# Kernel optimization log

Measured on AMD Instinct MI355X. Metric: run time of the kernel, lower is better.

## Reference

```python
import jax, jax.numpy as jnp
import numpy as np

LEAK = 0.01  # F.leaky_relu default negative_slope


def projection(p, cam, res):
    # Weak-perspective projection to normalized [-1,1] image coords.
    # cam = [s, tx, ty]; p [B,N,3] -> [B,N,2]
    s = cam[:, 0][:, None, None]
    t = cam[:, None, 1:3]
    return s * (p[..., :2] + t)


def grid_sample_points(im_feat, pts):
    # Bilinear grid_sample with align_corners=True, zeros padding,
    # specialized to a [B,N,1,2] point grid (matches points.unsqueeze(2)).
    # im_feat [B,C,H,W], pts [B,N,2] in [-1,1] -> [B,C,N]
    B, C, H, W = im_feat.shape
    N = pts.shape[1]
    x = (pts[..., 0] + 1.0) * 0.5 * (W - 1)
    y = (pts[..., 1] + 1.0) * 0.5 * (H - 1)
    x0 = jnp.floor(x)
    y0 = jnp.floor(y)
    x1 = x0 + 1.0
    y1 = y0 + 1.0
    wx1 = x - x0
    wx0 = 1.0 - wx1
    wy1 = y - y0
    wy0 = 1.0 - wy1
    feat_flat = im_feat.reshape(B, C, H * W)

    def gather(xi, yi, w):
        valid = (xi >= 0) & (xi <= W - 1) & (yi >= 0) & (yi <= H - 1)
        xc = jnp.clip(xi, 0, W - 1).astype(jnp.int32)
        yc = jnp.clip(yi, 0, H - 1).astype(jnp.int32)
        idx = (yc * W + xc)[:, None, :]  # [B,1,N]
        g = jnp.take_along_axis(feat_flat, jnp.broadcast_to(idx, (B, C, N)), axis=2)
        return g * (w * valid.astype(w.dtype))[:, None, :]

    return (gather(x0, y0, wx0 * wy0) + gather(x1, y0, wx1 * wy0)
            + gather(x0, y1, wx0 * wy1) + gather(x1, y1, wx1 * wy1))


def reduce_dim(feat, W0, b0, W1, b1, W2, b2):
    # feat [B,C0,N]; Conv1d kernel_size=1 == channel matmul.
    def conv1x1(x, W, b):
        return jnp.einsum('oc,bcn->bon', W, x) + b[None, :, None]

    y = jax.nn.leaky_relu(conv1x1(feat, W0, b0), LEAK)
    y = jax.nn.leaky_relu(conv1x1(jnp.concatenate([y, feat], axis=1), W1, b1), LEAK)
    y = conv1x1(jnp.concatenate([y, feat], axis=1), W2, b2)
    y = jax.nn.relu(y)  # last_op
    return y.reshape(y.shape[0], -1)  # [B, C_p*N]


def setup_inputs() -> dict:
    key = jax.random.key(0)
    ks = jax.random.split(key, 9)
    B, N, C, H, Wd = 64, 431, 256, 56, 56
    dims = [256, 128, 64, 5]
    p = jax.random.normal(ks[0], (B, N, 3), jnp.float32)
    cam = jax.random.uniform(ks[1], (B, 3), jnp.float32)
    s_feat = jax.random.normal(ks[2], (B, C, H, Wd), jnp.float32)
    W0 = jax.random.normal(ks[3], (dims[1], dims[0]), jnp.float32) * 0.02
    b0 = jnp.zeros((dims[1],), jnp.float32)
    W1 = jax.random.normal(ks[4], (dims[2], dims[1] + dims[0]), jnp.float32) * 0.02
    b1 = jnp.zeros((dims[2],), jnp.float32)
    W2 = jax.random.normal(ks[5], (dims[3], dims[2] + dims[0]), jnp.float32) * 0.02
    b2 = jnp.zeros((dims[3],), jnp.float32)
    return {"p": p, "cam": cam, "s_feat": s_feat,
            "W0": W0, "b0": b0, "W1": W1, "b1": b1, "W2": W2, "b2": b2,
            "res": 224}


def reference(p, cam, s_feat, W0, b0, W1, b1, W2, b2, res):
    p2d = projection(p, cam, res)                 # [B,N,2]
    point_feat = grid_sample_points(s_feat, p2d)  # [B,C_s,N]
    return reduce_dim(point_feat, W0, b0, W1, b1, W2, b2)  # [B, C_p*N]
```

## Files before the change

kernel.cpp:

```cpp
#include <hip/hip_runtime.h>


#define B_   64
#define N_   431
#define C_   256
#define H_   56
#define W_   56
#define HW_  3136
#define PPB  16
#define NT_  27
#define NPAD (NT_ * PPB)

#define Y0S  136
#define Y1S  72

typedef __attribute__((ext_vector_type(8))) short short8;
typedef __attribute__((ext_vector_type(4))) float f32x4;

__device__ __forceinline__ ushort f2bf(float f) {
    unsigned u = __float_as_uint(f);
    u += 0x7fffu + ((u >> 16) & 1u);
    return (ushort)(u >> 16);
}
__device__ __forceinline__ uint pack2(float lo, float hi) {
    return (uint)f2bf(lo) | ((uint)f2bf(hi) << 16);
}
__device__ __forceinline__ float lo16(uint u) { return __uint_as_float(u << 16); }
__device__ __forceinline__ float hi16(uint u) { return __uint_as_float(u & 0xffff0000u); }

#define WTOT (128 * 256 + 64 * 384 + 16 * 320)
#define GB_  (B_ * 64)

__global__ __launch_bounds__(256, 6) void gather_kernel(
    const float* __restrict__ p,
    const float* __restrict__ cam,
    const float* __restrict__ sfeat,
    const float* __restrict__ W0,
    const float* __restrict__ W1,
    const float* __restrict__ W2,
    ushort* __restrict__ feat,
    ushort* __restrict__ W0b,
    ushort* __restrict__ W1b,
    ushort* __restrict__ W2p)
{
    const int bx = blockIdx.x;
    if (bx >= GB_) {
        const int t0 = (bx - GB_) * 256 + threadIdx.x;
        for (int i = t0; i < WTOT; i += 8 * 256) {
            if (i < 128 * 256) {
                W0b[i] = f2bf(W0[i]);
            } else if (i < 128 * 256 + 64 * 384) {
                const int j = i - 128 * 256;
                W1b[j] = f2bf(W1[j]);
            } else {
                const int j = i - (128 * 256 + 64 * 384);
                const int r = j / 320, c = j - r * 320;
                W2p[j] = (r < 5) ? f2bf(W2[r * 320 + c]) : (ushort)0;
            }
        }
        return;
    }

    __shared__ uint plane01[HW_];
    __shared__ uint plane23[HW_];

    const int b  = bx >> 6;
    const int cg = bx & 63;
    const int c0 = cg * 4;
    const int t  = threadIdx.x;

    {
        const float4* __restrict__ s0 = (const float4*)(sfeat + ((size_t)b * C_ + c0 + 0) * HW_);
        const float4* __restrict__ s1 = (const float4*)(sfeat + ((size_t)b * C_ + c0 + 1) * HW_);
        const float4* __restrict__ s2 = (const float4*)(sfeat + ((size_t)b * C_ + c0 + 2) * HW_);
        const float4* __restrict__ s3 = (const float4*)(sfeat + ((size_t)b * C_ + c0 + 3) * HW_);
        for (int k = t; k < HW_ / 4; k += 256) {
            const float4 a = s0[k], bb = s1[k];
            uint4 u01;
            u01.x = pack2(a.x, bb.x); u01.y = pack2(a.y, bb.y);
            u01.z = pack2(a.z, bb.z); u01.w = pack2(a.w, bb.w);
            *(uint4*)&plane01[k * 4] = u01;
            const float4 c = s2[k], d = s3[k];
            uint4 u23;
            u23.x = pack2(c.x, d.x); u23.y = pack2(c.y, d.y);
            u23.z = pack2(c.z, d.z); u23.w = pack2(c.w, d.w);
            *(uint4*)&plane23[k * 4] = u23;
        }
    }
    __syncthreads();

    const float s  = cam[b * 3 + 0];
    const float tx = cam[b * 3 + 1];
    const float ty = cam[b * 3 + 2];
    ushort* __restrict__ fdst = feat + ((size_t)b * 64 + cg) * NPAD * 4;

    for (int n = t; n < NPAD; n += 256) {
        int   i00 = 0, i10 = 0, i01 = 0, i11 = 0;
        float w00 = 0.f, w10 = 0.f, w01 = 0.f, w11 = 0.f;
        if (n < N_) {
            const float px = p[((size_t)b * N_ + n) * 3 + 0];
            const float py = p[((size_t)b * N_ + n) * 3 + 1];
            const float x = (s * (px + tx) + 1.f) * 0.5f * (float)(W_ - 1);
            const float y = (s * (py + ty) + 1.f) * 0.5f * (float)(H_ - 1);
            const float x0f = floorf(x), y0f = floorf(y);
            const float wx1 = x - x0f, wx0 = 1.f - wx1;
            const float wy1 = y - y0f, wy0 = 1.f - wy1;
            const int ix0 = (int)x0f, iy0 = (int)y0f;
            const int ix1 = ix0 + 1,  iy1 = iy0 + 1;
            const bool vx0 = (ix0 >= 0) & (ix0 <= W_ - 1);
            const bool vx1 = (ix1 >= 0) & (ix1 <= W_ - 1);
            const bool vy0 = (iy0 >= 0) & (iy0 <= H_ - 1);
            const bool vy1 = (iy1 >= 0) & (iy1 <= H_ - 1);
            const int cx0 = min(max(ix0, 0), W_ - 1);
            const int cx1 = min(max(ix1, 0), W_ - 1);
            const int cy0 = min(max(iy0, 0), H_ - 1);
            const int cy1 = min(max(iy1, 0), H_ - 1);
            w00 = (vx0 & vy0) ? wx0 * wy0 : 0.f;
            w10 = (vx1 & vy0) ? wx1 * wy0 : 0.f;
            w01 = (vx0 & vy1) ? wx0 * wy1 : 0.f;
            w11 = (vx1 & vy1) ? wx1 * wy1 : 0.f;
            i00 = cy0 * W_ + cx0;  i10 = cy0 * W_ + cx1;
            i01 = cy1 * W_ + cx0;  i11 = cy1 * W_ + cx1;
        }
        const uint a00 = plane01[i00], a10 = plane01[i10], a01 = plane01[i01], a11 = plane01[i11];
        const uint c00 = plane23[i00], c10 = plane23[i10], c01 = plane23[i01], c11 = plane23[i11];
        const float v0 = w00 * lo16(a00) + w10 * lo16(a10) + w01 * lo16(a01) + w11 * lo16(a11);
        const float v1 = w00 * hi16(a00) + w10 * hi16(a10) + w01 * hi16(a01) + w11 * hi16(a11);
        const float v2 = w00 * lo16(c00) + w10 * lo16(c10) + w01 * lo16(c01) + w11 * lo16(c11);
        const float v3 = w00 * hi16(c00) + w10 * hi16(c10) + w01 * hi16(c01) + w11 * hi16(c11);
        ushort4 r;
        r.x = f2bf(v0); r.y = f2bf(v1); r.z = f2bf(v2); r.w = f2bf(v3);
        *(ushort4*)(fdst + (size_t)n * 4) = r;
    }
}

__global__ __launch_bounds__(256, 4) void mlp_kernel(
    const ushort* __restrict__ feat,
    const ushort* __restrict__ W0b,
    const float* __restrict__ b0,
    const ushort* __restrict__ W1b,
    const float* __restrict__ b1,
    const ushort* __restrict__ W2p,
    const float* __restrict__ b2,
    float* __restrict__ out)
{
    __shared__ ushort y0_s[PPB * Y0S];
    __shared__ ushort y1_s[PPB * Y1S];

    const int tid  = threadIdx.x;
    const int w    = tid >> 6;
    const int l    = tid & 63;
    const int m    = l & 15;
    const int q    = l >> 4;
    const int tile = blockIdx.x;
    const int b    = blockIdx.y;
    const int n0   = tile * PPB;
    const int n    = n0 + m;

    const ushort* __restrict__ fb = feat + (size_t)b * 64 * NPAD * 4;
    short8 af[8];
    #pragma unroll
    for (int ks = 0; ks < 8; ++ks) {
        const int cg0 = 8 * ks + 2 * q;
        union { short8 v; uint2 u[2]; } tmp;
        tmp.u[0] = *(const uint2*)(fb + ((size_t)cg0 * NPAD + n) * 4);
        tmp.u[1] = *(const uint2*)(fb + ((size_t)(cg0 + 1) * NPAD + n) * 4);
        af[ks] = tmp.v;
    }

    {
        f32x4 acc0 = {0.f, 0.f, 0.f, 0.f};
        f32x4 acc1 = {0.f, 0.f, 0.f, 0.f};
        const ushort* __restrict__ wr0 = W0b + ((size_t)(2 * w) * 16 + m) * 256 + 8 * q;
        const ushort* __restrict__ wr1 = wr0 + 16 * 256;
        #pragma unroll
        for (int ks = 0; ks < 8; ++ks) {
            const short8 w0 = *(const short8*)(wr0 + 32 * ks);
            const short8 w1 = *(const short8*)(wr1 + 32 * ks);
            acc0 = __builtin_amdgcn_mfma_f32_16x16x32_bf16(af[ks], w0, acc0, 0, 0, 0);
            acc1 = __builtin_amdgcn_mfma_f32_16x16x32_bf16(af[ks], w1, acc1, 0, 0, 0);
        }
        const int o0 = (2 * w) * 16 + m, o1 = o0 + 16;
        const float bias0 = b0[o0], bias1 = b0[o1];
        #pragma unroll
        for (int r = 0; r < 4; ++r) {
            float v0 = acc0[r] + bias0; v0 = (v0 > 0.f) ? v0 : 0.01f * v0;
            float v1 = acc1[r] + bias1; v1 = (v1 > 0.f) ? v1 : 0.01f * v1;
            y0_s[(q * 4 + r) * Y0S + o0] = f2bf(v0);
            y0_s[(q * 4 + r) * Y0S + o1] = f2bf(v1);
        }
    }
    __syncthreads();

    {
        f32x4 acc = {0.f, 0.f, 0.f, 0.f};
        const ushort* __restrict__ wr = W1b + ((size_t)w * 16 + m) * 384 + 8 * q;
        #pragma unroll
        for (int ks = 0; ks < 4; ++ks) {
            const short8 a  = *(const short8*)(y0_s + m * Y0S + 32 * ks + 8 * q);
            const short8 bb = *(const short8*)(wr + 32 * ks);
            acc = __builtin_amdgcn_mfma_f32_16x16x32_bf16(a, bb, acc, 0, 0, 0);
        }
        #pragma unroll
        for (int ks = 4; ks < 12; ++ks) {
            const short8 bb = *(const short8*)(wr + 32 * ks);
            acc = __builtin_amdgcn_mfma_f32_16x16x32_bf16(af[ks - 4], bb, acc, 0, 0, 0);
        }
        const int o = w * 16 + m;
        const float bias = b1[o];
        #pragma unroll
        for (int r = 0; r < 4; ++r) {
            float v = acc[r] + bias; v = (v > 0.f) ? v : 0.01f * v;
            y1_s[(q * 4 + r) * Y1S + o] = f2bf(v);
        }
    }
    __syncthreads();

    if (w == 0) {
        f32x4 acc = {0.f, 0.f, 0.f, 0.f};
        const ushort* __restrict__ wr = W2p + (size_t)m * 320 + 8 * q;
        #pragma unroll
        for (int ks = 0; ks < 2; ++ks) {
            const short8 a  = *(const short8*)(y1_s + m * Y1S + 32 * ks + 8 * q);
            const short8 bb = *(const short8*)(wr + 32 * ks);
            acc = __builtin_amdgcn_mfma_f32_16x16x32_bf16(a, bb, acc, 0, 0, 0);
        }
        #pragma unroll
        for (int ks = 2; ks < 10; ++ks) {
            const short8 bb = *(const short8*)(wr + 32 * ks);
            acc = __builtin_amdgcn_mfma_f32_16x16x32_bf16(af[ks - 2], bb, acc, 0, 0, 0);
        }
        if (m < 5) {
            const float bias = b2[m];
            #pragma unroll
            for (int r = 0; r < 4; ++r) {
                const int nn = n0 + q * 4 + r;
                if (nn < N_) {
                    float v = acc[r] + bias;
                    out[((size_t)b * 5 + m) * N_ + nn] = (v > 0.f) ? v : 0.f;
                }
            }
        }
    }
}

__global__ __launch_bounds__(256, 4) void maf_fallback_kernel(
    const float* __restrict__ p, const float* __restrict__ cam,
    const float* __restrict__ sfeat,
    const float* __restrict__ W0, const float* __restrict__ b0,
    const float* __restrict__ W1, const float* __restrict__ b1,
    const float* __restrict__ W2, const float* __restrict__ b2,
    float* __restrict__ out)
{
    __shared__ float feat_s[PPB][C_ + 4];
    __shared__ float y0_s[PPB][128 + 4];
    __shared__ float y1_s[PPB][64 + 4];

    const int tid = threadIdx.x;
    const int b   = blockIdx.y;
    const int n0  = blockIdx.x * PPB;
    const float s  = cam[b * 3 + 0];
    const float tx = cam[b * 3 + 1];
    const float ty = cam[b * 3 + 2];
    {
        const int c = tid;
        const float* __restrict__ fb = sfeat + ((size_t)b * C_ + c) * HW_;
        for (int pp = 0; pp < PPB; ++pp) {
            const int n = n0 + pp;
            float val = 0.f;
            if (n < N_) {
                const float px = p[((size_t)b * N_ + n) * 3 + 0];
                const float py = p[((size_t)b * N_ + n) * 3 + 1];
                const float x = (s * (px + tx) + 1.f) * 0.5f * (float)(W_ - 1);
                const float y = (s * (py + ty) + 1.f) * 0.5f * (float)(H_ - 1);
                const float x0f = floorf(x), y0f = floorf(y);
                const float wx1 = x - x0f, wx0 = 1.f - wx1;
                const float wy1 = y - y0f, wy0 = 1.f - wy1;
                const int ix0 = (int)x0f, iy0 = (int)y0f;
                const int ix1 = ix0 + 1,  iy1 = iy0 + 1;
                const bool vx0 = (ix0 >= 0) & (ix0 <= W_ - 1);
                const bool vx1 = (ix1 >= 0) & (ix1 <= W_ - 1);
                const bool vy0 = (iy0 >= 0) & (iy0 <= H_ - 1);
                const bool vy1 = (iy1 >= 0) & (iy1 <= H_ - 1);
                const int cx0 = min(max(ix0, 0), W_ - 1);
                const int cx1 = min(max(ix1, 0), W_ - 1);
                const int cy0 = min(max(iy0, 0), H_ - 1);
                const int cy1 = min(max(iy1, 0), H_ - 1);
                const float w00 = (vx0 & vy0) ? wx0 * wy0 : 0.f;
                const float w10 = (vx1 & vy0) ? wx1 * wy0 : 0.f;
                const float w01 = (vx0 & vy1) ? wx0 * wy1 : 0.f;
                const float w11 = (vx1 & vy1) ? wx1 * wy1 : 0.f;
                val = w00 * fb[cy0 * W_ + cx0] + w10 * fb[cy0 * W_ + cx1]
                    + w01 * fb[cy1 * W_ + cx0] + w11 * fb[cy1 * W_ + cx1];
            }
            feat_s[pp][c] = val;
        }
    }
    __syncthreads();
    {
        const int o = tid & 127, pg = tid >> 7, p0 = pg * 8;
        const float* __restrict__ wr = W0 + (size_t)o * 256;
        float acc[8] = {0, 0, 0, 0, 0, 0, 0, 0};
        for (int k = 0; k < 256; k += 4) {
            const float4 w = *(const float4*)(wr + k);
            for (int i = 0; i < 8; ++i) {
                const float4 f = *(const float4*)&feat_s[p0 + i][k];
                acc[i] += w.x * f.x + w.y * f.y + w.z * f.z + w.w * f.w;
            }
        }
        const float bias = b0[o];
        for (int i = 0; i < 8; ++i) {
            const float v = acc[i] + bias;
            y0_s[p0 + i][o] = (v > 0.f) ? v : 0.01f * v;
        }
    }
    __syncthreads();
    {
        const int o = tid & 63, pg = tid >> 6, p0 = pg * 4;
        const float* __restrict__ wr = W1 + (size_t)o * 384;
        float acc[4] = {0, 0, 0, 0};
        for (int k = 0; k < 128; k += 4) {
            const float4 w = *(const float4*)(wr + k);
            for (int i = 0; i < 4; ++i) {
                const float4 f = *(const float4*)&y0_s[p0 + i][k];
                acc[i] += w.x * f.x + w.y * f.y + w.z * f.z + w.w * f.w;
            }
        }
        for (int k = 0; k < 256; k += 4) {
            const float4 w = *(const float4*)(wr + 128 + k);
            for (int i = 0; i < 4; ++i) {
                const float4 f = *(const float4*)&feat_s[p0 + i][k];
                acc[i] += w.x * f.x + w.y * f.y + w.z * f.z + w.w * f.w;
            }
        }
        const float bias = b1[o];
        for (int i = 0; i < 4; ++i) {
            const float v = acc[i] + bias;
            y1_s[p0 + i][o] = (v > 0.f) ? v : 0.01f * v;
        }
    }
    __syncthreads();
    if (tid < 80) {
        const int o = tid >> 4, pp = tid & 15;
        const float* __restrict__ wr = W2 + (size_t)o * 320;
        float acc = 0.f;
        for (int k = 0; k < 64; k += 4) {
            const float4 w = *(const float4*)(wr + k);
            const float4 f = *(const float4*)&y1_s[pp][k];
            acc += w.x * f.x + w.y * f.y + w.z * f.z + w.w * f.w;
        }
        for (int k = 0; k < 256; k += 4) {
            const float4 w = *(const float4*)(wr + 64 + k);
            const float4 f = *(const float4*)&feat_s[pp][k];
            acc += w.x * f.x + w.y * f.y + w.z * f.z + w.w * f.w;
        }
        const int n = n0 + pp;
        if (n < N_) {
            float v = acc + b2[o];
            out[((size_t)b * 5 + o) * N_ + n] = (v > 0.f) ? v : 0.f;
        }
    }
}

extern "C" void kernel_launch(void* const* d_in, const int* in_sizes, int n_in,
                              void* d_out, int out_size, void* d_ws, size_t ws_size,
                              hipStream_t stream) {
    const float* p     = (const float*)d_in[0];
    const float* cam   = (const float*)d_in[1];
    const float* sfeat = (const float*)d_in[2];
    const float* W0    = (const float*)d_in[3];
    const float* b0    = (const float*)d_in[4];
    const float* W1    = (const float*)d_in[5];
    const float* b1    = (const float*)d_in[6];
    const float* W2    = (const float*)d_in[7];
    const float* b2    = (const float*)d_in[8];
    float* out = (float*)d_out;

    const size_t feat_elems = (size_t)B_ * 64 * NPAD * 4;
    size_t off = feat_elems;
    const size_t w0_off = off; off += 128 * 256;
    const size_t w1_off = off; off += 64 * 384;
    const size_t w2_off = off; off += 16 * 320;
    const size_t need = off * sizeof(ushort);

    if (ws_size >= need) {
        ushort* feat = (ushort*)d_ws;
        ushort* W0b  = feat + w0_off;
        ushort* W1b  = feat + w1_off;
        ushort* W2p  = feat + w2_off;
        gather_kernel<<<GB_ + 8, 256, 0, stream>>>(
            p, cam, sfeat, W0, W1, W2, feat, W0b, W1b, W2p);
        mlp_kernel<<<dim3(NT_, B_), 256, 0, stream>>>(
            feat, W0b, b0, W1b, b1, W2p, b2, out);
    } else {
        maf_fallback_kernel<<<dim3(NT_, B_), 256, 0, stream>>>(
            p, cam, sfeat, W0, b0, W1, b1, W2, b2, out);
    }
}
```

Measured before the change: 336.7 us.

## Process 32 points per MLP block and interleave channel-pair feature layout

The MLP kernel now handles 32 points per block instead of 16, so each wave reuses every loaded weight fragment across two MFMA point tiles and the grid shrinks from 27 to 14 tiles per batch. The gathered feature buffer is re-laid out so two channel groups are interleaved per point, letting each lane load a full 16-byte short8 fragment instead of two 8-byte pieces. The aim is to cut weight-load traffic and the number of global load instructions. The cost is more register pressure (launch bounds lowered to 3 waves per SIMD), fewer blocks, and some padding waste in the last tile.

```diff
diff --git a/kernel.cpp b/kernel.cpp
--- a/kernel.cpp
+++ b/kernel.cpp
@@ -9,7 +9,9 @@
 #define HW_  3136
 #define PPB  16
 #define NT_  27
-#define NPAD (NT_ * PPB)
+#define PPB2 32
+#define NT2  14
+#define NPAD (NT2 * PPB2)
 
 #define Y0S  136
 #define Y1S  72
@@ -92,7 +94,8 @@
     const float s  = cam[b * 3 + 0];
     const float tx = cam[b * 3 + 1];
     const float ty = cam[b * 3 + 2];
-    ushort* __restrict__ fdst = feat + ((size_t)b * 64 + cg) * NPAD * 4;
+    ushort* __restrict__ fdst = feat + ((size_t)b * 32 + (cg >> 1)) * NPAD * 8
+                                     + (size_t)(cg & 1) * 4;
 
     for (int n = t; n < NPAD; n += 256) {
         int   i00 = 0, i10 = 0, i01 = 0, i11 = 0;
@@ -130,11 +133,11 @@
         const float v3 = w00 * hi16(c00) + w10 * hi16(c10) + w01 * hi16(c01) + w11 * hi16(c11);
         ushort4 r;
         r.x = f2bf(v0); r.y = f2bf(v1); r.z = f2bf(v2); r.w = f2bf(v3);
-        *(ushort4*)(fdst + (size_t)n * 4) = r;
-    }
-}
-
-__global__ __launch_bounds__(256, 4) void mlp_kernel(
+        *(ushort4*)(fdst + (size_t)n * 8) = r;
+    }
+}
+
+__global__ __launch_bounds__(256, 3) void mlp_kernel(
     const ushort* __restrict__ feat,
     const ushort* __restrict__ W0b,
     const float* __restrict__ b0,
@@ -144,8 +147,8 @@
     const float* __restrict__ b2,
     float* __restrict__ out)
 {
-    __shared__ ushort y0_s[PPB * Y0S];
-    __shared__ ushort y1_s[PPB * Y1S];
+    __shared__ ushort y0_s[PPB2 * Y0S];
+    __shared__ ushort y1_s[PPB2 * Y1S];
 
     const int tid  = threadIdx.x;
     const int w    = tid >> 6;
@@ -154,87 +157,102 @@
     const int q    = l >> 4;
     const int tile = blockIdx.x;
     const int b    = blockIdx.y;
-    const int n0   = tile * PPB;
-    const int n    = n0 + m;
-
-    const ushort* __restrict__ fb = feat + (size_t)b * 64 * NPAD * 4;
-    short8 af[8];
+    const int n0   = tile * PPB2;
+
+    const ushort* __restrict__ fb = feat + (size_t)b * 32 * NPAD * 8;
+    short8 af0[8], af1[8];
     #pragma unroll
     for (int ks = 0; ks < 8; ++ks) {
-        const int cg0 = 8 * ks + 2 * q;
-        union { short8 v; uint2 u[2]; } tmp;
-        tmp.u[0] = *(const uint2*)(fb + ((size_t)cg0 * NPAD + n) * 4);
-        tmp.u[1] = *(const uint2*)(fb + ((size_t)(cg0 + 1) * NPAD + n) * 4);
-        af[ks] = tmp.v;
-    }
-
-    {
-        f32x4 acc0 = {0.f, 0.f, 0.f, 0.f};
-        f32x4 acc1 = {0.f, 0.f, 0.f, 0.f};
+        const size_t row = (size_t)(4 * ks + q) * NPAD;
+        af0[ks] = *(const short8*)(fb + (row + (n0 + m)) * 8);
+        af1[ks] = *(const short8*)(fb + (row + (n0 + 16 + m)) * 8);
+    }
+
+    {
+        f32x4 a00 = {0.f, 0.f, 0.f, 0.f};
+        f32x4 a01 = {0.f, 0.f, 0.f, 0.f};
+        f32x4 a10 = {0.f, 0.f, 0.f, 0.f};
+        f32x4 a11 = {0.f, 0.f, 0.f, 0.f};
         const ushort* __restrict__ wr0 = W0b + ((size_t)(2 * w) * 16 + m) * 256 + 8 * q;
         const ushort* __restrict__ wr1 = wr0 + 16 * 256;
         #pragma unroll
         for (int ks = 0; ks < 8; ++ks) {
             const short8 w0 = *(const short8*)(wr0 + 32 * ks);
             const short8 w1 = *(const short8*)(wr1 + 32 * ks);
-            acc0 = __builtin_amdgcn_mfma_f32_16x16x32_bf16(af[ks], w0, acc0, 0, 0, 0);
-            acc1 = __builtin_amdgcn_mfma_f32_16x16x32_bf16(af[ks], w1, acc1, 0, 0, 0);
+            a00 = __builtin_amdgcn_mfma_f32_16x16x32_bf16(af0[ks], w0, a00, 0, 0, 0);
+            a01 = __builtin_amdgcn_mfma_f32_16x16x32_bf16(af0[ks], w1, a01, 0, 0, 0);
+            a10 = __builtin_amdgcn_mfma_f32_16x16x32_bf16(af1[ks], w0, a10, 0, 0, 0);
+            a11 = __builtin_amdgcn_mfma_f32_16x16x32_bf16(af1[ks], w1, a11, 0, 0, 0);
         }
         const int o0 = (2 * w) * 16 + m, o1 = o0 + 16;
         const float bias0 = b0[o0], bias1 = b0[o1];
         #pragma unroll
         for (int r = 0; r < 4; ++r) {
-            float v0 = acc0[r] + bias0; v0 = (v0 > 0.f) ? v0 : 0.01f * v0;
-            float v1 = acc1[r] + bias1; v1 = (v1 > 0.f) ? v1 : 0.01f * v1;
-            y0_s[(q * 4 + r) * Y0S + o0] = f2bf(v0);
-            y0_s[(q * 4 + r) * Y0S + o1] = f2bf(v1);
-        }
-    }
-    __syncthreads();
-
-    {
+            float v;
+            v = a00[r] + bias0; v = (v > 0.f) ? v : 0.01f * v;
+            y0_s[(q * 4 + r) * Y0S + o0] = f2bf(v);
+            v = a01[r] + bias1; v = (v > 0.f) ? v : 0.01f * v;
+            y0_s[(q * 4 + r) * Y0S + o1] = f2bf(v);
+            v = a10[r] + bias0; v = (v > 0.f) ? v : 0.01f * v;
+            y0_s[(16 + q * 4 + r) * Y0S + o0] = f2bf(v);
+            v = a11[r] + bias1; v = (v > 0.f) ? v : 0.01f * v;
+            y0_s[(16 + q * 4 + r) * Y0S + o1] = f2bf(v);
+        }
+    }
+    __syncthreads();
+
+    {
+        f32x4 acc0 = {0.f, 0.f, 0.f, 0.f};
+        f32x4 acc1 = {0.f, 0.f, 0.f, 0.f};
+        const ushort* __restrict__ wr = W1b + ((size_t)w * 16 + m) * 384 + 8 * q;
+        #pragma unroll
+        for (int ks = 0; ks < 4; ++ks) {
+            const short8 a0 = *(const short8*)(y0_s + m * Y0S + 32 * ks + 8 * q);
+            const short8 a1 = *(const short8*)(y0_s + (16 + m) * Y0S + 32 * ks + 8 * q);
+            const short8 bb = *(const short8*)(wr + 32 * ks);
+            acc0 = __builtin_amdgcn_mfma_f32_16x16x32_bf16(a0, bb, acc0, 0, 0, 0);
+            acc1 = __builtin_amdgcn_mfma_f32_16x16x32_bf16(a1, bb, acc1, 0, 0, 0);
+        }
+        #pragma unroll
+        for (int ks = 4; ks < 12; ++ks) {
+            const short8 bb = *(const short8*)(wr + 32 * ks);
+            acc0 = __builtin_amdgcn_mfma_f32_16x16x32_bf16(af0[ks - 4], bb, acc0, 0, 0, 0);
+            acc1 = __builtin_amdgcn_mfma_f32_16x16x32_bf16(af1[ks - 4], bb, acc1, 0, 0, 0);
+        }
+        const int o = w * 16 + m;
+        const float bias = b1[o];
+        #pragma unroll
+        for (int r = 0; r < 4; ++r) {
+            float v;
+            v = acc0[r] + bias; v = (v > 0.f) ? v : 0.01f * v;
+            y1_s[(q * 4 + r) * Y1S + o] = f2bf(v);
+            v = acc1[r] + bias; v = (v > 0.f) ? v : 0.01f * v;
+            y1_s[(16 + q * 4 + r) * Y1S + o] = f2bf(v);
+        }
+    }
+    __syncthreads();
+
+    if (w < 2) {
+        const int mt = w;
         f32x4 acc = {0.f, 0.f, 0.f, 0.f};
-        const ushort* __restrict__ wr = W1b + ((size_t)w * 16 + m) * 384 + 8 * q;
-        #pragma unroll
-        for (int ks = 0; ks < 4; ++ks) {
-            const short8 a  = *(const short8*)(y0_s + m * Y0S + 32 * ks + 8 * q);
+        const ushort* __restrict__ wr = W2p + (size_t)m * 320 + 8 * q;
+        #pragma unroll
+        for (int ks = 0; ks < 2; ++ks) {
+            const short8 a  = *(const short8*)(y1_s + (mt * 16 + m) * Y1S + 32 * ks + 8 * q);
             const short8 bb = *(const short8*)(wr + 32 * ks);
             acc = __builtin_amdgcn_mfma_f32_16x16x32_bf16(a, bb, acc, 0, 0, 0);
         }
         #pragma unroll
-        for (int ks = 4; ks < 12; ++ks) {
-            const short8 bb = *(const short8*)(wr + 32 * ks);
-            acc = __builtin_amdgcn_mfma_f32_16x16x32_bf16(af[ks - 4], bb, acc, 0, 0, 0);
-        }
-        const int o = w * 16 + m;
-        const float bias = b1[o];
-        #pragma unroll
-        for (int r = 0; r < 4; ++r) {
-            float v = acc[r] + bias; v = (v > 0.f) ? v : 0.01f * v;
-            y1_s[(q * 4 + r) * Y1S + o] = f2bf(v);
-        }
-    }
-    __syncthreads();
-
-    if (w == 0) {
-        f32x4 acc = {0.f, 0.f, 0.f, 0.f};
-        const ushort* __restrict__ wr = W2p + (size_t)m * 320 + 8 * q;
-        #pragma unroll
-        for (int ks = 0; ks < 2; ++ks) {
-            const short8 a  = *(const short8*)(y1_s + m * Y1S + 32 * ks + 8 * q);
-            const short8 bb = *(const short8*)(wr + 32 * ks);
-            acc = __builtin_amdgcn_mfma_f32_16x16x32_bf16(a, bb, acc, 0, 0, 0);
-        }
-        #pragma unroll
         for (int ks = 2; ks < 10; ++ks) {
             const short8 bb = *(const short8*)(wr + 32 * ks);
-            acc = __builtin_amdgcn_mfma_f32_16x16x32_bf16(af[ks - 2], bb, acc, 0, 0, 0);
+            const short8 a  = mt ? af1[ks - 2] : af0[ks - 2];
+            acc = __builtin_amdgcn_mfma_f32_16x16x32_bf16(a, bb, acc, 0, 0, 0);
         }
         if (m < 5) {
             const float bias = b2[m];
             #pragma unroll
             for (int r = 0; r < 4; ++r) {
-                const int nn = n0 + q * 4 + r;
+                const int nn = n0 + mt * 16 + q * 4 + r;
                 if (nn < N_) {
                     float v = acc[r] + bias;
                     out[((size_t)b * 5 + m) * N_ + nn] = (v > 0.f) ? v : 0.f;
@@ -376,7 +394,7 @@
     const float* b2    = (const float*)d_in[8];
     float* out = (float*)d_out;
 
-    const size_t feat_elems = (size_t)B_ * 64 * NPAD * 4;
+    const size_t feat_elems = (size_t)B_ * 32 * NPAD * 8;
     size_t off = feat_elems;
     const size_t w0_off = off; off += 128 * 256;
     const size_t w1_off = off; off += 64 * 384;
@@ -390,7 +408,7 @@
         ushort* W2p  = feat + w2_off;
         gather_kernel<<<GB_ + 8, 256, 0, stream>>>(
             p, cam, sfeat, W0, W1, W2, feat, W0b, W1b, W2p);
-        mlp_kernel<<<dim3(NT_, B_), 256, 0, stream>>>(
+        mlp_kernel<<<dim3(NT2, B_), 256, 0, stream>>>(
             feat, W0b, b0, W1b, b1, W2p, b2, out);
     } else {
         maf_fallback_kernel<<<dim3(NT_, B_), 256, 0, stream>>>(
```

Result: faster. 330.0 us (-2.0%).
